# Performance work log

Hardware: AMD Instinct MI355X
Metric: run time of the kernel (lower is better)

The kernel has to match this reference:

```python
import jax, jax.numpy as jnp
import numpy as np

# Module config (matches init_kwargs)
DIM = 256
NUM_HEADS = 8
KS = (7, 7)            # kernel_sizes per split
DIL = (1, 2)           # dilations per split
NUM_SPLITS = 2
HEADS_PER = NUM_HEADS // NUM_SPLITS  # clean partition: 4 heads per split


def _nb_indices(L, ks, dil):
    """NATTEN neighborhood start + relative-position-bias indices along one axis.
    Each residue class (i % dil) is an independent 1D sequence; the k-window is
    clamped (shifted) at the borders exactly as in NATTEN's get_window_start.
    Returns nb [L, ks] key indices and bi [L, ks] rpb indices in [0, 2ks-2].
    """
    i = jnp.arange(L)
    r = i % dil
    p = i // dil
    Lr = (L - r + dil - 1) // dil              # length of residue class
    ps = jnp.clip(p - ks // 2, 0, Lr - ks)     # window start (subsampled coords)
    a = jnp.arange(ks)
    nb = (ps[:, None] + a[None, :]) * dil + r[:, None]   # [L, ks]
    bi = a[None, :] + (ps - p)[:, None] + (ks - 1)       # [L, ks]
    return nb, bi


def _na_split(q, k, v, rpb, ks, dil):
    """natten2dqkrpb -> softmax -> natten2dav for one head-group.
    q pre-scaled. q/k/v: [B,h,H,W,hd], rpb: [h,2ks-1,2ks-1]."""
    H, W = q.shape[2], q.shape[3]
    hn, hb = _nb_indices(H, ks, dil)
    wn, wb = _nb_indices(W, ks, dil)
    # gather local windows: [B,h,H,W,ks,ks,hd]
    kg = k[:, :, hn[:, None, :, None], wn[None, :, None, :], :]
    vg = v[:, :, hn[:, None, :, None], wn[None, :, None, :], :]
    attn = jnp.einsum('bhijd,bhijkld->bhijkl', q, kg)
    attn = attn + rpb[:, hb[:, None, :, None], wb[None, :, None, :]][None]  # [B,h,H,W,ks,ks]
    B, h = attn.shape[0], attn.shape[1]
    attn = jax.nn.softmax(attn.reshape(B, h, H, W, ks * ks), axis=-1)
    attn = attn.reshape(B, h, H, W, ks, ks)
    return jnp.einsum('bhijkl,bhijkld->bhijd', attn, vg)


def _forward(x, w_qkv, b_qkv, w_proj, b_proj, rpb0, rpb1):
    B, H, W, C = x.shape
    hd = C // NUM_HEADS
    scale = hd ** -0.5
    qkv = (x @ w_qkv + b_qkv).reshape(B, H, W, 3, NUM_HEADS, hd)
    qkv = jnp.transpose(qkv, (3, 0, 4, 1, 2, 5))  # [3,B,nh,H,W,hd]
    q, k, v = qkv[0] * scale, qkv[1], qkv[2]
    outs = []
    for s, rpb in enumerate((rpb0, rpb1)):
        sl = slice(s * HEADS_PER, (s + 1) * HEADS_PER)
        outs.append(_na_split(q[:, sl], k[:, sl], v[:, sl], rpb, KS[s], DIL[s]))
    out = jnp.concatenate(outs, axis=1)                      # [B,nh,H,W,hd]
    out = jnp.transpose(out, (0, 2, 3, 1, 4)).reshape(B, H, W, C)
    return out @ w_proj + b_proj


def setup_inputs() -> dict:
    key = jax.random.key(0)
    ks = jax.random.split(key, 6)
    C = DIM
    x = jax.random.normal(ks[0], (2, 56, 56, C), jnp.float32)
    w_qkv = jax.random.normal(ks[1], (C, 3 * C), jnp.float32) * 0.02
    b_qkv = jnp.zeros((3 * C,), jnp.float32)
    w_proj = jax.random.normal(ks[2], (C, C), jnp.float32) * 0.02
    b_proj = jnp.zeros((C,), jnp.float32)
    rpb0 = jax.random.normal(ks[3], (HEADS_PER, 2 * KS[0] - 1, 2 * KS[0] - 1), jnp.float32) * 0.02
    rpb1 = jax.random.normal(ks[4], (HEADS_PER, 2 * KS[1] - 1, 2 * KS[1] - 1), jnp.float32) * 0.02
    return {'x': x, 'w_qkv': w_qkv, 'b_qkv': b_qkv, 'w_proj': w_proj,
            'b_proj': b_proj, 'rpb0': rpb0, 'rpb1': rpb1}


def reference(x, w_qkv, b_qkv, w_proj, b_proj, rpb0, rpb1):
    return _forward(x, w_qkv, b_qkv, w_proj, b_proj, rpb0, rpb1)
```

## Files before the change

kernel.cpp:

```cpp
#include <hip/hip_runtime.h>
#include <stdint.h>

typedef __bf16 bf16_t;
typedef bf16_t bf16x8 __attribute__((ext_vector_type(8)));
typedef bf16_t bf16x2 __attribute__((ext_vector_type(2)));
typedef float floatx4 __attribute__((ext_vector_type(4)));

#define HW 56
#define NTOK 6272

__device__ __forceinline__ uint16_t f2bf(float f){
  union { float f; uint32_t i; } c; c.f = f;
  uint32_t r = (c.i + 0x7FFFu + ((c.i >> 16) & 1u)) >> 16;
  return (uint16_t)r;
}
__device__ __forceinline__ float bflo(uint32_t u){
  union { uint32_t i; float f; } c; c.i = u << 16; return c.f;
}
__device__ __forceinline__ float bfhi(uint32_t u){
  union { uint32_t i; float f; } c; c.i = u & 0xffff0000u; return c.f;
}

__device__ __forceinline__ float bdot2(uint32_t ka, uint32_t qa, float acc){
#if __has_builtin(__builtin_amdgcn_fdot2_f32_bf16)
  union { uint32_t u; bf16x2 v; } A, B;
  A.u = ka; B.u = qa;
  return __builtin_amdgcn_fdot2_f32_bf16(A.v, B.v, acc, false);
#else
  return acc + bflo(ka) * bflo(qa) + bfhi(ka) * bfhi(qa);
#endif
}

typedef __attribute__((address_space(1))) const void* gptr_t;
typedef __attribute__((address_space(3))) void* lptr_t;


__global__ __launch_bounds__(256) void prep_kernel(
    const float* __restrict__ x,      uint16_t* __restrict__ xb,
    const float* __restrict__ w_qkv,  uint16_t* __restrict__ wqkvT,
    const float* __restrict__ w_proj, uint16_t* __restrict__ wprojT)
{
  __shared__ uint16_t tile[64][65];
  const int bx = blockIdx.x;
  const int t = threadIdx.x;
  if (bx < 784){
    int idx = bx * 256 + t;
    const float4* s = (const float4*)x + (size_t)idx * 2;
    float4 a = s[0], b = s[1];
    uint4 pk;
    pk.x = (uint32_t)f2bf(a.x) | ((uint32_t)f2bf(a.y) << 16);
    pk.y = (uint32_t)f2bf(a.z) | ((uint32_t)f2bf(a.w) << 16);
    pk.z = (uint32_t)f2bf(b.x) | ((uint32_t)f2bf(b.y) << 16);
    pk.w = (uint32_t)f2bf(b.z) | ((uint32_t)f2bf(b.w) << 16);
    ((uint4*)xb)[idx] = pk;
    return;
  }
  const float* src; uint16_t* dst; int N, q;
  if (bx < 832){ q = bx - 784; src = w_qkv;  dst = wqkvT;  N = 768; }
  else         { q = bx - 832; src = w_proj; dst = wprojT; N = 256; }
  const int k0 = (q & 3) * 64, n0 = (q >> 2) * 64;
  for (int idx = t; idx < 64 * 64; idx += 256){
    int r = idx >> 6, c = idx & 63;
    tile[r][c] = f2bf(src[(k0 + r) * N + n0 + c]);
  }
  __syncthreads();
  for (int idx = t; idx < 64 * 64; idx += 256){
    int r = idx >> 6, c = idx & 63;
    dst[(n0 + r) * 256 + k0 + c] = tile[c][r];
  }
}

#define KDIM 256
#define KHALF 128

template<int OUTF32, int AHM, int NT>
__global__ __launch_bounds__(512, 2) void gemm_bt_bias(
    const uint16_t* __restrict__ A,
    const uint16_t* __restrict__ Bt,
    const float* __restrict__ bias,
    void* __restrict__ Cv,
    int N)
{
  constexpr int NF = NT / 32;
  __shared__ __align__(16) uint16_t Al[128 * KHALF];
  __shared__ __align__(16) uint16_t Bl[NT * KHALF];
  const int m0 = blockIdx.x * 128, n0 = blockIdx.y * NT;
  const int t = threadIdx.x;
  const int lane = t & 63;
  const int wave = t >> 6;
  const int wm = (wave & 3) * 32;
  const int wn = (wave >> 2) * (NF * 16);
  const int fr = lane & 15;

  floatx4 acc[2][NF];
  #pragma unroll
  for (int mi = 0; mi < 2; mi++)
    #pragma unroll
    for (int nf = 0; nf < NF; nf++) acc[mi][nf] = (floatx4){0.f,0.f,0.f,0.f};

  constexpr int AGRP = 4;
  constexpr int BGRP = NT / 32;

  for (int ko = 0; ko < 2; ko++){
    if (ko) __syncthreads();
    #pragma unroll
    for (int gg = 0; gg < AGRP; gg++){
      int g = wave + gg * 8;
      int L = g * 64 + lane;
      int row = L >> 4, cs = L & 15;
      int cg = cs ^ (row & 15);
      const uint16_t* ga;
      if (AHM){
        int d0 = ko * KHALF + cg * 8;
        ga = A + (size_t)(d0 >> 5) * (NTOK * 32) + (m0 + row) * 32 + (d0 & 31);
      } else {
        ga = A + (size_t)(m0 + row) * KDIM + ko * KHALF + cg * 8;
      }
      __builtin_amdgcn_global_load_lds((gptr_t)ga, (lptr_t)(Al + g * 512), 16, 0, 0);
    }
    #pragma unroll
    for (int gg = 0; gg < BGRP; gg++){
      int g = wave + gg * 8;
      int L = g * 64 + lane;
      int row = L >> 4, cs = L & 15;
      int cg = cs ^ (row & 15);
      const uint16_t* gb = Bt + (size_t)(n0 + row) * KDIM + ko * KHALF + cg * 8;
      __builtin_amdgcn_global_load_lds((gptr_t)gb, (lptr_t)(Bl + g * 512), 16, 0, 0);
    }
    __syncthreads();
    #pragma unroll
    for (int kk = 0; kk < KHALF; kk += 32){
      const int sel = ((((kk >> 3) + (lane >> 4)) ^ fr) << 3);
      bf16x8 a0 = *(const bf16x8*)(Al + (wm + fr)      * KHALF + sel);
      bf16x8 a1 = *(const bf16x8*)(Al + (wm + 16 + fr) * KHALF + sel);
      bf16x8 bfrag[NF];
      #pragma unroll
      for (int nf = 0; nf < NF; nf++)
        bfrag[nf] = *(const bf16x8*)(Bl + (wn + nf * 16 + fr) * KHALF + sel);
      #pragma unroll
      for (int nf = 0; nf < NF; nf++){
        acc[0][nf] = __builtin_amdgcn_mfma_f32_16x16x32_bf16(a0, bfrag[nf], acc[0][nf], 0, 0, 0);
        acc[1][nf] = __builtin_amdgcn_mfma_f32_16x16x32_bf16(a1, bfrag[nf], acc[1][nf], 0, 0, 0);
      }
    }
  }

  const int ccol = lane & 15;
  const int crow = (lane >> 4) * 4;
  float bv[NF];
  #pragma unroll
  for (int nf = 0; nf < NF; nf++) bv[nf] = bias[n0 + wn + nf * 16 + ccol];
  #pragma unroll
  for (int mi = 0; mi < 2; mi++){
    #pragma unroll
    for (int r2 = 0; r2 < 4; r2++){
      int r = m0 + wm + mi * 16 + crow + r2;
      #pragma unroll
      for (int nf = 0; nf < NF; nf++){
        int cidx = r * N + n0 + wn + nf * 16 + ccol;
        if (OUTF32) ((float*)Cv)[cidx] = acc[mi][nf][r2] + bv[nf];
        else        ((uint16_t*)Cv)[cidx] = f2bf(acc[mi][nf][r2] + bv[nf]);
      }
    }
  }
}

#define WIN 20
#define PPL 3200

__global__ __launch_bounds__(256, 3) void natten_kernel(
    const uint16_t* __restrict__ qkv,
    const float* __restrict__ rpb0,
    const float* __restrict__ rpb1,
    uint16_t* __restrict__ attnH)
{
  __shared__ uint16_t KS[400 * 32];
  __shared__ uint16_t VS[4 * PPL];
  __shared__ float RPB[169];

  const int t = threadIdx.x;
  const int z = blockIdx.x;
  const int b = z >> 3, h = z & 7;
  const int j0 = blockIdx.y * 8, i0 = blockIdx.z * 8;
  const int split = h >> 2;
  const int dil = split + 1;
  const float* rpb = (split ? rpb1 : rpb0) + (h & 3) * 169;
  if (t < 169) RPB[t] = rpb[t];

  const int r0 = max(0, i0 - 3 * dil);
  const int c0 = max(0, j0 - 3 * dil);
  const int R  = min(55, i0 + 7 + 3 * dil) - r0 + 1;
  const int C  = min(55, j0 + 7 + 3 * dil) - c0 + 1;

  const int nchunk = R * WIN * 4;
  for (int ch = t; ch < nchunk; ch += 256){
    int tok = ch >> 2, q = ch & 3;
    int tr = tok / WIN;
    int tc = tok - tr * WIN;
    if (tc < C){
      const uint16_t* src = qkv + (size_t)((b * HW + r0 + tr) * HW + c0 + tc) * 768
                            + 256 + h * 32 + q * 8;
      int kl = tok * 32 + ((q ^ (tok & 3) ^ ((tok >> 2) & 3)) << 3);
      *(bf16x8*)(KS + kl) = *(const bf16x8*)(src);
      int vl = q * PPL + ((tok ^ ((5 * q) & 7)) << 3);
      *(bf16x8*)(VS + vl) = *(const bf16x8*)(src + 256);
    }
  }
  __syncthreads();

  const int c  = t & 3;
  const int qi = t >> 2;
  const int j = j0 + (qi & 7);
  const int i = i0 + (qi >> 3);

  const int ri = i % dil, pi = i / dil;
  const int rj = j % dil, pj = j / dil;
  const int Lri = (HW - ri + dil - 1) / dil;
  const int Lrj = (HW - rj + dil - 1) / dil;
  const int psi = min(max(pi - 3, 0), Lri - 7);
  const int psj = min(max(pj - 3, 0), Lrj - 7);
  const int bi0 = psi - pi + 6, bj0 = psj - pj + 6;
  const int ni0 = psi * dil + ri, nj0 = psj * dil + rj;

  const int tok = (b * HW + i) * HW + j;
  const float scale = 0.17677669529663687f;

  uint32_t qp[16];
  {
    const uint16_t* qsrc = qkv + (size_t)tok * 768 + h * 32;
    uint4 u0 = *(const uint4*)(qsrc);
    uint4 u1 = *(const uint4*)(qsrc + 8);
    uint4 u2 = *(const uint4*)(qsrc + 16);
    uint4 u3 = *(const uint4*)(qsrc + 24);
    qp[0]  = u0.x; qp[1]  = u0.y; qp[2]  = u0.z; qp[3]  = u0.w;
    qp[4]  = u1.x; qp[5]  = u1.y; qp[6]  = u1.z; qp[7]  = u1.w;
    qp[8]  = u2.x; qp[9]  = u2.y; qp[10] = u2.z; qp[11] = u2.w;
    qp[12] = u3.x; qp[13] = u3.y; qp[14] = u3.z; qp[15] = u3.w;
  }

  const int lbase = (ni0 - r0) * WIN + (nj0 - c0);

  float lgl[13];
  #pragma unroll
  for (int m = 0; m < 13; m++){
    int a = 4 * m + c;
    const bool valid = (a <= 48);
    if (!valid) a = 48;
    int ai = a / 7;
    int aj = a - ai * 7;
    int tk = lbase + (ai * WIN + aj) * dil;
    const int tswz = ((tk & 3) ^ ((tk >> 2) & 3));
    float dacc = 0.f;
    #pragma unroll
    for (int cc = 0; cc < 4; cc++){
      uint4 u = *(const uint4*)(KS + tk * 32 + ((cc ^ tswz) << 3));
      dacc = bdot2(u.x, qp[cc * 4 + 0], dacc);
      dacc = bdot2(u.y, qp[cc * 4 + 1], dacc);
      dacc = bdot2(u.z, qp[cc * 4 + 2], dacc);
      dacc = bdot2(u.w, qp[cc * 4 + 3], dacc);
    }
    float d = dacc * scale + RPB[(bi0 + ai) * 13 + (bj0 + aj)];
    lgl[m] = valid ? d : -1e30f;
  }

  float mx = lgl[0];
  #pragma unroll
  for (int s = 1; s < 13; s++) mx = fmaxf(mx, lgl[s]);
  mx = fmaxf(mx, __shfl_xor(mx, 1));
  mx = fmaxf(mx, __shfl_xor(mx, 2));
  float ssum = 0.f;
  #pragma unroll
  for (int s = 0; s < 13; s++){
    float e = __expf(lgl[s] - mx);
    lgl[s] = e;
    ssum += e;
  }
  ssum += __shfl_xor(ssum, 1);
  ssum += __shfl_xor(ssum, 2);
  float inv = 1.0f / ssum;

  float ov[8];
  #pragma unroll
  for (int d = 0; d < 8; d++) ov[d] = 0.f;

  const int cpl = c * PPL;
  const int cx  = (5 * c) & 7;
  const int lane4 = t & 60;
  #pragma unroll
  for (int ai = 0; ai < 7; ai++){
    int lrow = lbase + ai * dil * WIN;
    #pragma unroll
    for (int aj = 0; aj < 7; aj++){
      const int a = ai * 7 + aj;
      int tk = lrow + aj * dil;
      uint4 u = *(const uint4*)(VS + cpl + ((tk ^ cx) << 3));
      float w = __shfl(lgl[a >> 2], lane4 | (a & 3)) * inv;
      ov[0] += w * bflo(u.x); ov[1] += w * bfhi(u.x);
      ov[2] += w * bflo(u.y); ov[3] += w * bfhi(u.y);
      ov[4] += w * bflo(u.z); ov[5] += w * bfhi(u.z);
      ov[6] += w * bflo(u.w); ov[7] += w * bfhi(u.w);
    }
  }

  uint4 pk;
  pk.x = (uint32_t)f2bf(ov[0]) | ((uint32_t)f2bf(ov[1]) << 16);
  pk.y = (uint32_t)f2bf(ov[2]) | ((uint32_t)f2bf(ov[3]) << 16);
  pk.z = (uint32_t)f2bf(ov[4]) | ((uint32_t)f2bf(ov[5]) << 16);
  pk.w = (uint32_t)f2bf(ov[6]) | ((uint32_t)f2bf(ov[7]) << 16);
  *(uint4*)(attnH + ((size_t)h * NTOK + tok) * 32 + c * 8) = pk;
}

extern "C" void kernel_launch(void* const* d_in, const int* in_sizes, int n_in,
                              void* d_out, int out_size, void* d_ws, size_t ws_size,
                              hipStream_t stream)
{
  (void)in_sizes; (void)n_in; (void)out_size; (void)ws_size;
  const float* x      = (const float*)d_in[0];
  const float* w_qkv  = (const float*)d_in[1];
  const float* b_qkv  = (const float*)d_in[2];
  const float* w_proj = (const float*)d_in[3];
  const float* b_proj = (const float*)d_in[4];
  const float* rpb0   = (const float*)d_in[5];
  const float* rpb1   = (const float*)d_in[6];
  float* out = (float*)d_out;

  uint16_t* wqkvT  = (uint16_t*)d_ws;
  uint16_t* wprojT = wqkvT + 768 * 256;
  uint16_t* xb     = wprojT + 256 * 256;
  uint16_t* qkv    = xb + (size_t)NTOK * 256;
  uint16_t* attn   = qkv + (size_t)NTOK * 768;

  prep_kernel<<<dim3(848), 256, 0, stream>>>(x, xb, w_qkv, wqkvT, w_proj, wprojT);
  gemm_bt_bias<0, 0, 128><<<dim3(49, 6), 512, 0, stream>>>(xb, wqkvT, b_qkv, qkv, 768);
  natten_kernel<<<dim3(16, 7, 7), 256, 0, stream>>>(qkv, rpb0, rpb1, attn);
  gemm_bt_bias<1, 1, 64><<<dim3(49, 4), 512, 0, stream>>>(attn, wprojT, b_proj, out, 256);
}
```

Before: 103.4 us.

## Fuse x bf16 conversion into QKV GEMM and restructure natten AV accumulation

The separate x-to-bf16 conversion pass is removed. The QKV GEMM now reads fp32 x directly, converts it in registers and stores it swizzled into LDS, which avoids one full activation write and read. The natten AV stage changes from each lane accumulating 8 channels over all 49 neighbours to each lane accumulating all 32 channels over its own 13 neighbours, followed by a butterfly shuffle reduction. V now shares the K LDS layout. This removes the per-neighbour weight shuffles but costs more registers and turns the GEMM A-load into synchronous global loads.

```diff
diff --git a/kernel.cpp b/kernel.cpp
--- a/kernel.cpp
+++ b/kernel.cpp
@@ -35,29 +35,16 @@
 typedef __attribute__((address_space(3))) void* lptr_t;
 
 
-__global__ __launch_bounds__(256) void prep_kernel(
-    const float* __restrict__ x,      uint16_t* __restrict__ xb,
+__global__ __launch_bounds__(256) void prep_w_kernel(
     const float* __restrict__ w_qkv,  uint16_t* __restrict__ wqkvT,
     const float* __restrict__ w_proj, uint16_t* __restrict__ wprojT)
 {
   __shared__ uint16_t tile[64][65];
   const int bx = blockIdx.x;
   const int t = threadIdx.x;
-  if (bx < 784){
-    int idx = bx * 256 + t;
-    const float4* s = (const float4*)x + (size_t)idx * 2;
-    float4 a = s[0], b = s[1];
-    uint4 pk;
-    pk.x = (uint32_t)f2bf(a.x) | ((uint32_t)f2bf(a.y) << 16);
-    pk.y = (uint32_t)f2bf(a.z) | ((uint32_t)f2bf(a.w) << 16);
-    pk.z = (uint32_t)f2bf(b.x) | ((uint32_t)f2bf(b.y) << 16);
-    pk.w = (uint32_t)f2bf(b.z) | ((uint32_t)f2bf(b.w) << 16);
-    ((uint4*)xb)[idx] = pk;
-    return;
-  }
   const float* src; uint16_t* dst; int N, q;
-  if (bx < 832){ q = bx - 784; src = w_qkv;  dst = wqkvT;  N = 768; }
-  else         { q = bx - 832; src = w_proj; dst = wprojT; N = 256; }
+  if (bx < 48){ q = bx;      src = w_qkv;  dst = wqkvT;  N = 768; }
+  else        { q = bx - 48; src = w_proj; dst = wprojT; N = 256; }
   const int k0 = (q & 3) * 64, n0 = (q >> 2) * 64;
   for (int idx = t; idx < 64 * 64; idx += 256){
     int r = idx >> 6, c = idx & 63;
@@ -73,9 +60,9 @@
 #define KDIM 256
 #define KHALF 128
 
-template<int OUTF32, int AHM, int NT>
+template<int OUTF32, int AHM, int NT, int AF32>
 __global__ __launch_bounds__(512, 2) void gemm_bt_bias(
-    const uint16_t* __restrict__ A,
+    const void* __restrict__ Av,
     const uint16_t* __restrict__ Bt,
     const float* __restrict__ bias,
     void* __restrict__ Cv,
@@ -104,21 +91,6 @@
   for (int ko = 0; ko < 2; ko++){
     if (ko) __syncthreads();
     #pragma unroll
-    for (int gg = 0; gg < AGRP; gg++){
-      int g = wave + gg * 8;
-      int L = g * 64 + lane;
-      int row = L >> 4, cs = L & 15;
-      int cg = cs ^ (row & 15);
-      const uint16_t* ga;
-      if (AHM){
-        int d0 = ko * KHALF + cg * 8;
-        ga = A + (size_t)(d0 >> 5) * (NTOK * 32) + (m0 + row) * 32 + (d0 & 31);
-      } else {
-        ga = A + (size_t)(m0 + row) * KDIM + ko * KHALF + cg * 8;
-      }
-      __builtin_amdgcn_global_load_lds((gptr_t)ga, (lptr_t)(Al + g * 512), 16, 0, 0);
-    }
-    #pragma unroll
     for (int gg = 0; gg < BGRP; gg++){
       int g = wave + gg * 8;
       int L = g * 64 + lane;
@@ -126,6 +98,32 @@
       int cg = cs ^ (row & 15);
       const uint16_t* gb = Bt + (size_t)(n0 + row) * KDIM + ko * KHALF + cg * 8;
       __builtin_amdgcn_global_load_lds((gptr_t)gb, (lptr_t)(Bl + g * 512), 16, 0, 0);
+    }
+    #pragma unroll
+    for (int gg = 0; gg < AGRP; gg++){
+      int g = wave + gg * 8;
+      int L = g * 64 + lane;
+      int row = L >> 4, cs = L & 15;
+      if (AF32){
+        const float* ga = (const float*)Av + (size_t)(m0 + row) * KDIM + ko * KHALF + cs * 8;
+        float4 f0 = *(const float4*)ga;
+        float4 f1 = *(const float4*)(ga + 4);
+        bf16x8 v;
+        v[0] = (bf16_t)f0.x; v[1] = (bf16_t)f0.y; v[2] = (bf16_t)f0.z; v[3] = (bf16_t)f0.w;
+        v[4] = (bf16_t)f1.x; v[5] = (bf16_t)f1.y; v[6] = (bf16_t)f1.z; v[7] = (bf16_t)f1.w;
+        int slot = row * 16 + (cs ^ (row & 15));
+        *(bf16x8*)(Al + slot * 8) = v;
+      } else {
+        int cg = cs ^ (row & 15);
+        const uint16_t* ga;
+        if (AHM){
+          int d0 = ko * KHALF + cg * 8;
+          ga = (const uint16_t*)Av + (size_t)(d0 >> 5) * (NTOK * 32) + (m0 + row) * 32 + (d0 & 31);
+        } else {
+          ga = (const uint16_t*)Av + (size_t)(m0 + row) * KDIM + ko * KHALF + cg * 8;
+        }
+        __builtin_amdgcn_global_load_lds((gptr_t)ga, (lptr_t)(Al + g * 512), 16, 0, 0);
+      }
     }
     __syncthreads();
     #pragma unroll
@@ -166,7 +164,6 @@
 }
 
 #define WIN 20
-#define PPL 3200
 
 __global__ __launch_bounds__(256, 3) void natten_kernel(
     const uint16_t* __restrict__ qkv,
@@ -175,7 +172,7 @@
     uint16_t* __restrict__ attnH)
 {
   __shared__ uint16_t KS[400 * 32];
-  __shared__ uint16_t VS[4 * PPL];
+  __shared__ uint16_t VS[400 * 32];
   __shared__ float RPB[169];
 
   const int t = threadIdx.x;
@@ -202,8 +199,7 @@
                             + 256 + h * 32 + q * 8;
       int kl = tok * 32 + ((q ^ (tok & 3) ^ ((tok >> 2) & 3)) << 3);
       *(bf16x8*)(KS + kl) = *(const bf16x8*)(src);
-      int vl = q * PPL + ((tok ^ ((5 * q) & 7)) << 3);
-      *(bf16x8*)(VS + vl) = *(const bf16x8*)(src + 256);
+      *(bf16x8*)(VS + kl) = *(const bf16x8*)(src + 256);
     }
   }
   __syncthreads();
@@ -279,34 +275,53 @@
   ssum += __shfl_xor(ssum, 2);
   float inv = 1.0f / ssum;
 
-  float ov[8];
-  #pragma unroll
-  for (int d = 0; d < 8; d++) ov[d] = 0.f;
-
-  const int cpl = c * PPL;
-  const int cx  = (5 * c) & 7;
-  const int lane4 = t & 60;
-  #pragma unroll
-  for (int ai = 0; ai < 7; ai++){
-    int lrow = lbase + ai * dil * WIN;
-    #pragma unroll
-    for (int aj = 0; aj < 7; aj++){
-      const int a = ai * 7 + aj;
-      int tk = lrow + aj * dil;
-      uint4 u = *(const uint4*)(VS + cpl + ((tk ^ cx) << 3));
-      float w = __shfl(lgl[a >> 2], lane4 | (a & 3)) * inv;
-      ov[0] += w * bflo(u.x); ov[1] += w * bfhi(u.x);
-      ov[2] += w * bflo(u.y); ov[3] += w * bfhi(u.y);
-      ov[4] += w * bflo(u.z); ov[5] += w * bfhi(u.z);
-      ov[6] += w * bflo(u.w); ov[7] += w * bfhi(u.w);
-    }
+  float ov[32];
+  #pragma unroll
+  for (int d = 0; d < 32; d++) ov[d] = 0.f;
+
+  #pragma unroll
+  for (int m = 0; m < 13; m++){
+    int a = 4 * m + c;
+    if (a > 48) a = 48;
+    int ai = a / 7;
+    int aj = a - ai * 7;
+    int tk = lbase + (ai * WIN + aj) * dil;
+    const int tswz = ((tk & 3) ^ ((tk >> 2) & 3));
+    float w = lgl[m] * inv;
+    #pragma unroll
+    for (int cc = 0; cc < 4; cc++){
+      uint4 u = *(const uint4*)(VS + tk * 32 + ((cc ^ tswz) << 3));
+      ov[cc * 8 + 0] += w * bflo(u.x); ov[cc * 8 + 1] += w * bfhi(u.x);
+      ov[cc * 8 + 2] += w * bflo(u.y); ov[cc * 8 + 3] += w * bfhi(u.y);
+      ov[cc * 8 + 4] += w * bflo(u.z); ov[cc * 8 + 5] += w * bfhi(u.z);
+      ov[cc * 8 + 6] += w * bflo(u.w); ov[cc * 8 + 7] += w * bfhi(u.w);
+    }
+  }
+
+  float ovn[16];
+  #pragma unroll
+  for (int k = 0; k < 16; k++){
+    int da = (k < 8) ? k : (8 + k);
+    int db = (k < 8) ? (8 + k) : (16 + k);
+    float send = (c & 1) ? ov[da] : ov[db];
+    float recv = __shfl_xor(send, 1);
+    float keep = (c & 1) ? ov[db] : ov[da];
+    ovn[k] = keep + recv;
+  }
+  float ovf[8];
+  #pragma unroll
+  for (int k = 0; k < 8; k++){
+    float send = (c & 2) ? ovn[k] : ovn[k + 8];
+    float recv = __shfl_xor(send, 2);
+    float keep = (c & 2) ? ovn[k + 8] : ovn[k];
+    ovf[k] = keep + recv;
   }
 
   uint4 pk;
-  pk.x = (uint32_t)f2bf(ov[0]) | ((uint32_t)f2bf(ov[1]) << 16);
-  pk.y = (uint32_t)f2bf(ov[2]) | ((uint32_t)f2bf(ov[3]) << 16);
-  pk.z = (uint32_t)f2bf(ov[4]) | ((uint32_t)f2bf(ov[5]) << 16);
-  pk.w = (uint32_t)f2bf(ov[6]) | ((uint32_t)f2bf(ov[7]) << 16);
+  pk.x = (uint32_t)f2bf(ovf[0]) | ((uint32_t)f2bf(ovf[1]) << 16);
+  pk.y = (uint32_t)f2bf(ovf[2]) | ((uint32_t)f2bf(ovf[3]) << 16);
+  pk.z = (uint32_t)f2bf(ovf[4]) | ((uint32_t)f2bf(ovf[5]) << 16);
+  pk.w = (uint32_t)f2bf(ovf[6]) | ((uint32_t)f2bf(ovf[7]) << 16);
   *(uint4*)(attnH + ((size_t)h * NTOK + tok) * 32 + c * 8) = pk;
 }
 
@@ -326,12 +341,11 @@
 
   uint16_t* wqkvT  = (uint16_t*)d_ws;
   uint16_t* wprojT = wqkvT + 768 * 256;
-  uint16_t* xb     = wprojT + 256 * 256;
-  uint16_t* qkv    = xb + (size_t)NTOK * 256;
+  uint16_t* qkv    = wprojT + 256 * 256;
   uint16_t* attn   = qkv + (size_t)NTOK * 768;
 
-  prep_kernel<<<dim3(848), 256, 0, stream>>>(x, xb, w_qkv, wqkvT, w_proj, wprojT);
-  gemm_bt_bias<0, 0, 128><<<dim3(49, 6), 512, 0, stream>>>(xb, wqkvT, b_qkv, qkv, 768);
+  prep_w_kernel<<<dim3(64), 256, 0, stream>>>(w_qkv, wqkvT, w_proj, wprojT);
+  gemm_bt_bias<0, 0, 128, 1><<<dim3(49, 6), 512, 0, stream>>>(x, wqkvT, b_qkv, qkv, 768);
   natten_kernel<<<dim3(16, 7, 7), 256, 0, stream>>>(qkv, rpb0, rpb1, attn);
-  gemm_bt_bias<1, 1, 64><<<dim3(49, 4), 512, 0, stream>>>(attn, wprojT, b_proj, out, 256);
-}
+  gemm_bt_bias<1, 1, 64, 0><<<dim3(49, 4), 512, 0, stream>>>(attn, wprojT, b_proj, out, 256);
+}
```

After: 195.9 us. 89.6% more time.
